# Optimization experiments

Hardware: AMD Instinct MI355X
Metric: run time of the kernel (lower is better)

The kernel has to match this reference:

```python
import jax, jax.numpy as jnp
import numpy as np


def setup_inputs() -> dict:
    key = jax.random.key(0)
    k1, k2 = jax.random.split(key)
    B, N, M, D = 4, 4096, 4096, 32
    x1 = jax.random.normal(k1, (B, N, D), dtype=jnp.float32)
    x2 = jax.random.normal(k2, (B, M, D), dtype=jnp.float32)
    const = jnp.ones((1,), dtype=jnp.float32)
    return {"x1": x1, "x2": x2, "const": const}


def reference(x1, x2, const):
    # Pairwise dot products: [B,N,D] x [B,M,D] -> [B,N,M], then add scalar bias.
    # (Original materializes an O(N*M*D) broadcast intermediate; einsum/bmm avoids it.)
    numerator = jnp.einsum("bnd,bmd->bnm", x1, x2)
    return numerator + const
```

## Files before the change

kernel.cpp:

```cpp
#include <hip/hip_runtime.h>


typedef _Float16 half8 __attribute__((ext_vector_type(8)));
typedef float    f32x4 __attribute__((ext_vector_type(4)));

constexpr int Bv = 4;
constexpr int Nv = 4096;
constexpr int Mv = 4096;
constexpr int Dv = 32;
constexpr int TM = 128;
constexpr int TN = 256;

__global__ __launch_bounds__(256, 2)
void pairwise_dot_bias_mfma(const float* __restrict__ x1,
                            const float* __restrict__ x2,
                            const float* __restrict__ cbias,
                            float* __restrict__ out) {
    const int b  = blockIdx.z;
    const int n0 = blockIdx.y * TM;
    const int m0 = blockIdx.x * TN;
    const int t  = threadIdx.x;
    const int w    = t >> 6;
    const int lane = t & 63;
    const int l16  = lane & 15;
    const int lh   = lane >> 4;

    const float* x1b = x1 + (size_t)b * Nv * Dv;
    const float* x2b = x2 + (size_t)b * Mv * Dv;
    const float  cb  = cbias[0];
    float* outb = out + (size_t)b * Nv * Mv;

    half8 afrag[8];
    #pragma unroll
    for (int rg = 0; rg < 8; ++rg) {
        const float* p = x1b + (size_t)(n0 + rg * 16 + l16) * Dv + lh * 8;
        const f32x4 f0 = *reinterpret_cast<const f32x4*>(p);
        const f32x4 f1 = *reinterpret_cast<const f32x4*>(p + 4);
        afrag[rg][0] = (_Float16)f0.x; afrag[rg][1] = (_Float16)f0.y;
        afrag[rg][2] = (_Float16)f0.z; afrag[rg][3] = (_Float16)f0.w;
        afrag[rg][4] = (_Float16)f1.x; afrag[rg][5] = (_Float16)f1.y;
        afrag[rg][6] = (_Float16)f1.z; afrag[rg][7] = (_Float16)f1.w;
    }

    #pragma unroll
    for (int c = 0; c < 4; ++c) {
        const int mcol = m0 + w * 64 + c * 16 + l16;
        const float* p = x2b + (size_t)mcol * Dv + lh * 8;
        const f32x4 g0 = *reinterpret_cast<const f32x4*>(p);
        const f32x4 g1 = *reinterpret_cast<const f32x4*>(p + 4);
        half8 bfrag;
        bfrag[0] = (_Float16)g0.x; bfrag[1] = (_Float16)g0.y;
        bfrag[2] = (_Float16)g0.z; bfrag[3] = (_Float16)g0.w;
        bfrag[4] = (_Float16)g1.x; bfrag[5] = (_Float16)g1.y;
        bfrag[6] = (_Float16)g1.z; bfrag[7] = (_Float16)g1.w;

        #pragma unroll
        for (int rg = 0; rg < 8; ++rg) {
            f32x4 acc = {0.f, 0.f, 0.f, 0.f};
            acc = __builtin_amdgcn_mfma_f32_16x16x32_f16(afrag[rg], bfrag, acc, 0, 0, 0);
            const int rbase = n0 + rg * 16 + lh * 4;
            #pragma unroll
            for (int r = 0; r < 4; ++r)
                outb[(size_t)(rbase + r) * Mv + mcol] = acc[r] + cb;
        }
    }
}

extern "C" void kernel_launch(void* const* d_in, const int* in_sizes, int n_in,
                              void* d_out, int out_size, void* d_ws, size_t ws_size,
                              hipStream_t stream) {
    const float* x1 = (const float*)d_in[0];
    const float* x2 = (const float*)d_in[1];
    const float* cb = (const float*)d_in[2];
    float* out = (float*)d_out;

    dim3 grid(Mv / TN, Nv / TM, Bv);
    pairwise_dot_bias_mfma<<<grid, 256, 0, stream>>>(x1, x2, cb, out);
}
```

Baseline: 68.88 us.

## Stage MFMA outputs through LDS for vectorized row-contiguous stores with thin row tiles

Each block now covers 16 rows and 2048 columns, and each wave walks 64-column panels. Accumulator tiles are transposed through a per-wave LDS buffer so every lane writes a 16-byte float4 along a row, instead of scattered 4-byte stores. The goal is to reduce the store-transaction cost of this write-bound kernel. In exchange, x2 is re-read and re-converted for every 16-row tile, and the kernel adds LDS traffic and the risk of bank conflicts.

```diff
diff --git a/kernel.cpp b/kernel.cpp
--- a/kernel.cpp
+++ b/kernel.cpp
@@ -8,18 +8,23 @@
 constexpr int Nv = 4096;
 constexpr int Mv = 4096;
 constexpr int Dv = 32;
-constexpr int TM = 128;
-constexpr int TN = 256;
+constexpr int TM = 16;
+constexpr int COLS_PER_BLOCK = 2048;
+constexpr int COLS_PER_WAVE  = 512;
+constexpr int NPANEL = COLS_PER_WAVE / 64;
+constexpr int LW = 68;
 
-__global__ __launch_bounds__(256, 2)
-void pairwise_dot_bias_mfma(const float* __restrict__ x1,
-                            const float* __restrict__ x2,
-                            const float* __restrict__ cbias,
-                            float* __restrict__ out) {
+__global__ __launch_bounds__(256)
+void pairwise_mfma_stream(const float* __restrict__ x1,
+                          const float* __restrict__ x2,
+                          const float* __restrict__ cbias,
+                          float* __restrict__ out) {
+    __shared__ float tbuf[4][TM][LW];
+
     const int b  = blockIdx.z;
     const int n0 = blockIdx.y * TM;
-    const int m0 = blockIdx.x * TN;
-    const int t  = threadIdx.x;
+    const int c0 = blockIdx.x * COLS_PER_BLOCK;
+    const int t    = threadIdx.x;
     const int w    = t >> 6;
     const int lane = t & 63;
     const int l16  = lane & 15;
@@ -30,38 +35,48 @@
     const float  cb  = cbias[0];
     float* outb = out + (size_t)b * Nv * Mv;
 
-    half8 afrag[8];
-    #pragma unroll
-    for (int rg = 0; rg < 8; ++rg) {
-        const float* p = x1b + (size_t)(n0 + rg * 16 + l16) * Dv + lh * 8;
-        const f32x4 f0 = *reinterpret_cast<const f32x4*>(p);
-        const f32x4 f1 = *reinterpret_cast<const f32x4*>(p + 4);
-        afrag[rg][0] = (_Float16)f0.x; afrag[rg][1] = (_Float16)f0.y;
-        afrag[rg][2] = (_Float16)f0.z; afrag[rg][3] = (_Float16)f0.w;
-        afrag[rg][4] = (_Float16)f1.x; afrag[rg][5] = (_Float16)f1.y;
-        afrag[rg][6] = (_Float16)f1.z; afrag[rg][7] = (_Float16)f1.w;
-    }
+    const float* pa = x1b + (size_t)(n0 + l16) * Dv + lh * 8;
+    const f32x4 a0 = *reinterpret_cast<const f32x4*>(pa);
+    const f32x4 a1 = *reinterpret_cast<const f32x4*>(pa + 4);
+    half8 af;
+    af[0] = (_Float16)a0.x; af[1] = (_Float16)a0.y;
+    af[2] = (_Float16)a0.z; af[3] = (_Float16)a0.w;
+    af[4] = (_Float16)a1.x; af[5] = (_Float16)a1.y;
+    af[6] = (_Float16)a1.z; af[7] = (_Float16)a1.w;
 
-    #pragma unroll
-    for (int c = 0; c < 4; ++c) {
-        const int mcol = m0 + w * 64 + c * 16 + l16;
-        const float* p = x2b + (size_t)mcol * Dv + lh * 8;
-        const f32x4 g0 = *reinterpret_cast<const f32x4*>(p);
-        const f32x4 g1 = *reinterpret_cast<const f32x4*>(p + 4);
-        half8 bfrag;
-        bfrag[0] = (_Float16)g0.x; bfrag[1] = (_Float16)g0.y;
-        bfrag[2] = (_Float16)g0.z; bfrag[3] = (_Float16)g0.w;
-        bfrag[4] = (_Float16)g1.x; bfrag[5] = (_Float16)g1.y;
-        bfrag[6] = (_Float16)g1.z; bfrag[7] = (_Float16)g1.w;
+    float (*buf)[LW] = tbuf[w];
+    const int colw = c0 + w * COLS_PER_WAVE;
+
+    for (int p = 0; p < NPANEL; ++p) {
+        const int colp = colw + p * 64;
+
+        f32x4 acc[4];
+        #pragma unroll
+        for (int c = 0; c < 4; ++c) {
+            const float* pb = x2b + (size_t)(colp + c * 16 + l16) * Dv + lh * 8;
+            const f32x4 b0 = *reinterpret_cast<const f32x4*>(pb);
+            const f32x4 b1 = *reinterpret_cast<const f32x4*>(pb + 4);
+            half8 bf;
+            bf[0] = (_Float16)b0.x; bf[1] = (_Float16)b0.y;
+            bf[2] = (_Float16)b0.z; bf[3] = (_Float16)b0.w;
+            bf[4] = (_Float16)b1.x; bf[5] = (_Float16)b1.y;
+            bf[6] = (_Float16)b1.z; bf[7] = (_Float16)b1.w;
+            f32x4 z = {0.f, 0.f, 0.f, 0.f};
+            acc[c] = __builtin_amdgcn_mfma_f32_16x16x32_f16(af, bf, z, 0, 0, 0);
+        }
 
         #pragma unroll
-        for (int rg = 0; rg < 8; ++rg) {
-            f32x4 acc = {0.f, 0.f, 0.f, 0.f};
-            acc = __builtin_amdgcn_mfma_f32_16x16x32_f16(afrag[rg], bfrag, acc, 0, 0, 0);
-            const int rbase = n0 + rg * 16 + lh * 4;
+        for (int c = 0; c < 4; ++c)
             #pragma unroll
             for (int r = 0; r < 4; ++r)
-                outb[(size_t)(rbase + r) * Mv + mcol] = acc[r] + cb;
+                buf[lh * 4 + r][c * 16 + l16] = acc[c][r];
+
+        #pragma unroll
+        for (int j = 0; j < 4; ++j) {
+            f32x4 v = *reinterpret_cast<const f32x4*>(&buf[j * 4 + lh][l16 * 4]);
+            v.x += cb; v.y += cb; v.z += cb; v.w += cb;
+            *reinterpret_cast<f32x4*>(
+                &outb[(size_t)(n0 + j * 4 + lh) * Mv + colp + l16 * 4]) = v;
         }
     }
 }
@@ -74,6 +89,6 @@
     const float* cb = (const float*)d_in[2];
     float* out = (float*)d_out;
 
-    dim3 grid(Mv / TN, Nv / TM, Bv);
-    pairwise_dot_bias_mfma<<<grid, 256, 0, stream>>>(x1, x2, cb, out);
+    dim3 grid(Mv / COLS_PER_BLOCK, Nv / TM, Bv);
+    pairwise_mfma_stream<<<grid, 256, 0, stream>>>(x1, x2, cb, out);
 }
```

Result: slower. 84.32 us (+22.4%).
